# Performance work log

Measured on AMD Instinct MI355X. Metric: run time of the kernel, lower is better.

## Reference

```python
import jax, jax.numpy as jnp
import numpy as np

B, S, HID, NH, DH, L, FF = 1, 4096, 768, 12, 64, 12, 3072
WIN = 256       # one-sided sliding window (attention_window = 512 total)
NG = 16         # number of global-attention tokens
VOCAB = 50265
NEG = -1e9


def layer_norm(x, g, b, eps=1e-5):
    mu = jnp.mean(x, -1, keepdims=True)
    var = jnp.mean((x - mu) ** 2, -1, keepdims=True)
    return (x - mu) * jax.lax.rsqrt(var + eps) * g + b


def forward(input_ids, attention_mask, global_attention_mask, tok_emb, pos_emb,
            emb_ln_w, emb_ln_b, Wqkv, bqkv, Wo, bo, ln1_w, ln1_b,
            W1, b1, W2, b2, ln2_w, ln2_b, cls_W, cls_b):
    c = WIN
    nc = S // c
    amask = attention_mask.astype(jnp.float32)          # [B,S]
    gmask = global_attention_mask.astype(jnp.float32)   # [B,S]

    # --- static-shape helpers for the sparse pattern ---
    # key chunk k covers padded positions [k*c, k*c + 3c)
    idx = (jnp.arange(nc) * c)[:, None] + jnp.arange(3 * c)[None, :]      # [nc,3c]
    diff = jnp.arange(3 * c)[None, :] - c - jnp.arange(c)[:, None]        # [c,3c]
    band = jnp.abs(diff) <= c
    mp = jnp.pad(amask, ((0, 0), (c, c)))[:, idx]                         # [B,nc,3c]
    gp = jnp.pad(gmask, ((0, 0), (c, c)))[:, idx]
    key_ok = (mp > 0) & (gp == 0)           # local keys: valid and not global (globals handled separately)
    loc_valid = band[None, None] & key_ok[:, :, None, :]                  # [B,nc,c,3c]

    # indices of the NG global tokens (earliest first)
    _, gidx = jax.lax.top_k(gmask * (2.0 * S) - jnp.arange(S, dtype=jnp.float32), NG)
    gvalid = jnp.take_along_axis(gmask, gidx, axis=1)                     # [B,NG]

    def attn(x, Wqkv_l, bqkv_l, Wo_l, bo_l):
        qkv = x @ Wqkv_l + bqkv_l
        q, k, v = jnp.split(qkv, 3, axis=-1)
        hd = lambda t: t.reshape(B, S, NH, DH).transpose(0, 2, 1, 3)      # [B,nh,S,dh]
        q = hd(q) * (DH ** -0.5); k = hd(k); v = hd(v)

        # sliding-window (banded) attention via overlapping key chunks
        kp = jnp.pad(k, ((0, 0), (0, 0), (c, c), (0, 0)))
        vp = jnp.pad(v, ((0, 0), (0, 0), (c, c), (0, 0)))
        Kc, Vc = kp[:, :, idx], vp[:, :, idx]                             # [B,nh,nc,3c,dh]
        Qc = q.reshape(B, NH, nc, c, DH)
        s_loc = jnp.einsum('bhkpd,bhkqd->bhkpq', Qc, Kc)                  # [B,nh,nc,c,3c]
        s_loc = jnp.where(loc_valid[:, None], s_loc, NEG)

        # every token also attends to the global tokens
        gi = jnp.broadcast_to(gidx[:, None, :, None], (B, NH, NG, DH))
        Kg = jnp.take_along_axis(k, gi, axis=2)                           # [B,nh,NG,dh]
        Vg = jnp.take_along_axis(v, gi, axis=2)
        Qg = jnp.take_along_axis(q, gi, axis=2)
        s_glb = jnp.einsum('bhkpd,bhgd->bhkpg', Qc, Kg)                   # [B,nh,nc,c,NG]
        s_glb = jnp.where(gvalid[:, None, None, None, :] > 0, s_glb, NEG)

        p = jax.nn.softmax(jnp.concatenate([s_loc, s_glb], -1), axis=-1)
        o = (jnp.einsum('bhkpq,bhkqd->bhkpd', p[..., :3 * c], Vc)
             + jnp.einsum('bhkpg,bhgd->bhkpd', p[..., 3 * c:], Vg))
        o = o.reshape(B, NH, S, DH).transpose(0, 2, 1, 3)                 # [B,S,nh,dh]

        # global tokens attend to the full sequence
        s_full = jnp.einsum('bhgd,bhsd->bhgs', Qg, k)
        s_full = jnp.where(amask[:, None, None, :] > 0, s_full, NEG)
        og = jnp.einsum('bhgs,bhsd->bhgd', jax.nn.softmax(s_full, -1), v)
        og = og.transpose(0, 2, 1, 3)                                     # [B,NG,nh,dh]
        bi = jnp.arange(B)[:, None]
        o = o.at[bi, gidx].set(jnp.where(gvalid[..., None, None] > 0, og, o[bi, gidx]))
        return o.reshape(B, S, HID) @ Wo_l + bo_l

    h = layer_norm(tok_emb[input_ids] + pos_emb[None], emb_ln_w, emb_ln_b)

    def step(h, p):
        Wq, bq, Wo_l, bo_l, g1, bl1, w1, bb1, w2, bb2, g2, bl2 = p
        h = layer_norm(h + attn(h, Wq, bq, Wo_l, bo_l), g1, bl1)          # post-LN, RoBERTa-style
        f = jax.nn.gelu(h @ w1 + bb1, approximate=False) @ w2 + bb2
        h = layer_norm(h + f, g2, bl2)
        return h, None

    h, _ = jax.lax.scan(step, h, (Wqkv, bqkv, Wo, bo, ln1_w, ln1_b,
                                  W1, b1, W2, b2, ln2_w, ln2_b))
    m = amask[..., None]
    pooled = (h * m).sum(1) / m.sum(1)           # masked mean-pool; dropout is eval no-op
    return pooled @ cls_W + cls_b                # [B,2] logits


def setup_inputs():
    key = jax.random.key(0)
    ks = jax.random.split(key, 8)
    nrm = lambda k, shp: jax.random.normal(k, shp, jnp.float32) * 0.02
    return dict(
        input_ids=jax.random.randint(ks[0], (B, S), 0, VOCAB),
        attention_mask=jnp.ones((B, S), jnp.int32),
        global_attention_mask=jnp.concatenate(
            [jnp.ones((B, NG), jnp.int32), jnp.zeros((B, S - NG), jnp.int32)], axis=1),
        tok_emb=nrm(ks[1], (VOCAB, HID)),
        pos_emb=nrm(ks[2], (S, HID)),
        emb_ln_w=jnp.ones((HID,)), emb_ln_b=jnp.zeros((HID,)),
        Wqkv=nrm(ks[3], (L, HID, 3 * HID)), bqkv=jnp.zeros((L, 3 * HID)),
        Wo=nrm(ks[4], (L, HID, HID)), bo=jnp.zeros((L, HID)),
        ln1_w=jnp.ones((L, HID)), ln1_b=jnp.zeros((L, HID)),
        W1=nrm(ks[5], (L, HID, FF)), b1=jnp.zeros((L, FF)),
        W2=nrm(ks[6], (L, FF, HID)), b2=jnp.zeros((L, HID)),
        ln2_w=jnp.ones((L, HID)), ln2_b=jnp.zeros((L, HID)),
        cls_W=nrm(ks[7], (HID, 2)), cls_b=jnp.zeros((2,)),
    )


def reference(input_ids, attention_mask, global_attention_mask, tok_emb, pos_emb,
              emb_ln_w, emb_ln_b, Wqkv, bqkv, Wo, bo, ln1_w, ln1_b,
              W1, b1, W2, b2, ln2_w, ln2_b, cls_W, cls_b):
    return forward(input_ids, attention_mask, global_attention_mask, tok_emb, pos_emb,
                   emb_ln_w, emb_ln_b, Wqkv, bqkv, Wo, bo, ln1_w, ln1_b,
                   W1, b1, W2, b2, ln2_w, ln2_b, cls_W, cls_b)
```

## Files before the change

### kernel.cpp

```cpp
#include <hip/hip_runtime.h>
#include <cmath>

#define S 4096
#define HID 768
#define NH 12
#define DH 64
#define CHUNK 256
#define NC (S / CHUNK)
#define NG 16
#define FF 3072
#define NLAYER 12
#define QKV3 (3 * HID)
#define NEGV -1e9f

typedef _Float16 f16;
typedef __attribute__((ext_vector_type(2))) _Float16 f16x2;
typedef __attribute__((ext_vector_type(4))) _Float16 f16x4;
typedef __attribute__((ext_vector_type(8))) _Float16 f16x8;
typedef __attribute__((ext_vector_type(4))) float f32x4;

__device__ __forceinline__ void async16(f16* lds, const f16* g) {
  __builtin_amdgcn_global_load_lds((const __attribute__((address_space(1))) unsigned int*)g,
                                   (__attribute__((address_space(3))) unsigned int*)lds,
                                   16, 0, 0);
}

__device__ __forceinline__ int xcd_swz(int lin, int nwg) {
  return (lin & 7) * (nwg >> 3) + (lin >> 3);
}

__device__ __forceinline__ float block_reduce_sum(float v, float* red) {
  int t = threadIdx.x;
  red[t] = v; __syncthreads();
  for (int st = 128; st > 0; st >>= 1) {
    if (t < st) red[t] += red[t + st];
    __syncthreads();
  }
  float r = red[0]; __syncthreads();
  return r;
}

__global__ void gidx_kernel(const int* __restrict__ gmask, int* __restrict__ gidx,
                            float* __restrict__ gvalid) {
  if (threadIdx.x != 0 || blockIdx.x != 0) return;
  int cnt = 0;
  for (int s = 0; s < S && cnt < NG; s++)
    if (gmask[s] > 0) { gidx[cnt] = s; gvalid[cnt] = 1.f; cnt++; }
  for (int s = 0; s < S && cnt < NG; s++)
    if (gmask[s] == 0) { gidx[cnt] = s; gvalid[cnt] = 0.f; cnt++; }
}

__global__ __launch_bounds__(256) void embed_ln_kernel(
    const int* __restrict__ ids, const float* __restrict__ tok,
    const float* __restrict__ pos, const float* __restrict__ g,
    const float* __restrict__ b, f16* __restrict__ h16) {
  int s = blockIdx.x, t = threadIdx.x;
  __shared__ float xs[HID];
  __shared__ float red[256];
  const float* tr = tok + (size_t)ids[s] * HID;
  const float* pr = pos + (size_t)s * HID;
  float ls = 0.f;
  for (int i = t; i < HID; i += 256) { float v = tr[i] + pr[i]; xs[i] = v; ls += v; }
  float mu = block_reduce_sum(ls, red) * (1.f / HID);
  float lv = 0.f;
  for (int i = t; i < HID; i += 256) { float d = xs[i] - mu; lv += d * d; }
  float var = block_reduce_sum(lv, red) * (1.f / HID);
  float inv = rsqrtf(var + 1e-5f);
  for (int i = t; i < HID; i += 256)
    h16[(size_t)s * HID + i] = (f16)((xs[i] - mu) * inv * g[i] + b[i]);
}

__global__ __launch_bounds__(256) void ln_kernel(
    const f16* __restrict__ sum16, const float* __restrict__ g,
    const float* __restrict__ b, f16* __restrict__ h16) {
  int s = blockIdx.x, t = threadIdx.x;
  __shared__ float red[256];
  float x[4] = {0.f, 0.f, 0.f, 0.f};
  if (t < 192) {
    f16x4 v = *(const f16x4*)&sum16[(size_t)s * HID + t * 4];
#pragma unroll
    for (int e = 0; e < 4; e++) x[e] = (float)v[e];
  }
  float mu = block_reduce_sum(x[0] + x[1] + x[2] + x[3], red) * (1.f / HID);
  float vs = 0.f;
  if (t < 192) {
#pragma unroll
    for (int e = 0; e < 4; e++) { float d = x[e] - mu; vs += d * d; }
  }
  float var = block_reduce_sum(vs, red) * (1.f / HID);
  float inv = rsqrtf(var + 1e-5f);
  if (t < 192) {
    float4 gv = *(const float4*)&g[t * 4];
    float4 bv = *(const float4*)&b[t * 4];
    f16x4 o;
    o[0] = (f16)((x[0] - mu) * inv * gv.x + bv.x);
    o[1] = (f16)((x[1] - mu) * inv * gv.y + bv.y);
    o[2] = (f16)((x[2] - mu) * inv * gv.z + bv.z);
    o[3] = (f16)((x[3] - mu) * inv * gv.w + bv.w);
    *(f16x4*)&h16[(size_t)s * HID + t * 4] = o;
  }
}

__global__ __launch_bounds__(256) void ln_ffn2_kernel(
    const f16* __restrict__ p0, const f16* __restrict__ p1,
    const float* __restrict__ bias, const float* __restrict__ g,
    const float* __restrict__ b, f16* __restrict__ h16) {
  int s = blockIdx.x, t = threadIdx.x;
  __shared__ float red[256];
  size_t base = (size_t)s * HID;
  float x[4] = {0.f, 0.f, 0.f, 0.f};
  if (t < 192) {
    f16x4 a = *(const f16x4*)&p0[base + t * 4];
    f16x4 c = *(const f16x4*)&p1[base + t * 4];
    f16x4 r = *(const f16x4*)&h16[base + t * 4];
    float4 bb = *(const float4*)&bias[t * 4];
    x[0] = (float)a[0] + (float)c[0] + bb.x + (float)r[0];
    x[1] = (float)a[1] + (float)c[1] + bb.y + (float)r[1];
    x[2] = (float)a[2] + (float)c[2] + bb.z + (float)r[2];
    x[3] = (float)a[3] + (float)c[3] + bb.w + (float)r[3];
  }
  float mu = block_reduce_sum(x[0] + x[1] + x[2] + x[3], red) * (1.f / HID);
  float vs = 0.f;
  if (t < 192) {
#pragma unroll
    for (int e = 0; e < 4; e++) { float d = x[e] - mu; vs += d * d; }
  }
  float var = block_reduce_sum(vs, red) * (1.f / HID);
  float inv = rsqrtf(var + 1e-5f);
  if (t < 192) {
    float4 gv = *(const float4*)&g[t * 4];
    float4 bv = *(const float4*)&b[t * 4];
    f16x4 o;
    o[0] = (f16)((x[0] - mu) * inv * gv.x + bv.x);
    o[1] = (f16)((x[1] - mu) * inv * gv.y + bv.y);
    o[2] = (f16)((x[2] - mu) * inv * gv.z + bv.z);
    o[3] = (f16)((x[3] - mu) * inv * gv.w + bv.w);
    *(f16x4*)&h16[base + t * 4] = o;
  }
}

__global__ __launch_bounds__(256) void wt_kernel(const float* __restrict__ W,
                                                 f16* __restrict__ WT, int K, int N) {
  size_t lo = (size_t)blockIdx.z * K * N;
  const float* Wl = W + lo;
  f16* WTl = WT + lo;
  __shared__ float tile[32][33];
  int k0 = blockIdx.y * 32, n0 = blockIdx.x * 32;
  int t = threadIdx.x;
  int r = t >> 3, c = (t & 7) * 4;
  float4 v = *(const float4*)&Wl[(size_t)(k0 + r) * N + n0 + c];
  tile[r][c] = v.x; tile[r][c + 1] = v.y; tile[r][c + 2] = v.z; tile[r][c + 3] = v.w;
  __syncthreads();
  int n = t >> 3, kq = (t & 7) * 4;
  f16x4 o = {(f16)tile[kq][n], (f16)tile[kq + 1][n], (f16)tile[kq + 2][n], (f16)tile[kq + 3][n]};
  *(f16x4*)&WTl[(size_t)(n0 + n) * K + k0 + kq] = o;
}

#define GBK 64

template <bool GELU>
__global__ __launch_bounds__(256) void gemm_f16_kernel(
    const f16* __restrict__ A, const f16* __restrict__ BT,
    const float* __restrict__ bias, f16* __restrict__ Cout, int M, int N, int K) {
  __shared__ f16 smem[17408];
  f16* As = smem;
  f16* Bs = smem + 8192;
  int t = threadIdx.x, lane = t & 63, wave = t >> 6;
  int wr = wave >> 1, wc = wave & 1;
  int gx = gridDim.x;
  int nl = xcd_swz(blockIdx.y * gx + blockIdx.x, gx * gridDim.y);
  int bx = nl % gx, by = nl / gx;

  f32x4 acc[4][4];
#pragma unroll
  for (int mi = 0; mi < 4; mi++)
#pragma unroll
    for (int ni = 0; ni < 4; ni++) acc[mi][ni] = (f32x4){0.f, 0.f, 0.f, 0.f};

  const f16* Ablk = A + (size_t)(by * 128) * K;
  const f16* Bblk = BT + (size_t)(bx * 128) * K;
  int rl = lane >> 3;
  int lc = (lane & 7) ^ rl;

  for (int k0 = 0; k0 < K; k0 += GBK) {
#pragma unroll
    for (int ii = 0; ii < 4; ii++) {
      int i = wave * 4 + ii;
      int r = i * 8 + rl;
      async16(&As[i * 512], Ablk + (size_t)r * K + k0 + lc * 8);
      async16(&Bs[i * 512], Bblk + (size_t)r * K + k0 + lc * 8);
    }
    __syncthreads();
#pragma unroll
    for (int kc = 0; kc < 2; kc++) {
      f16x8 af[4], bf[4];
#pragma unroll
      for (int mi = 0; mi < 4; mi++) {
        int row = wr * 64 + mi * 16 + (lane & 15);
        int pc = (kc * 4 + (lane >> 4)) ^ (row & 7);
        af[mi] = *(const f16x8*)&As[row * 64 + pc * 8];
      }
#pragma unroll
      for (int ni = 0; ni < 4; ni++) {
        int row = wc * 64 + ni * 16 + (lane & 15);
        int pc = (kc * 4 + (lane >> 4)) ^ (row & 7);
        bf[ni] = *(const f16x8*)&Bs[row * 64 + pc * 8];
      }
#pragma unroll
      for (int mi = 0; mi < 4; mi++)
#pragma unroll
        for (int ni = 0; ni < 4; ni++)
          acc[mi][ni] = __builtin_amdgcn_mfma_f32_16x16x32_f16(af[mi], bf[ni], acc[mi][ni], 0, 0, 0);
    }
    __syncthreads();
  }

  f16* Cs = smem;
  int rloc = wr * 64 + (lane >> 4) * 4;
  int cloc = wc * 64 + (lane & 15);
#pragma unroll
  for (int mi = 0; mi < 4; mi++) {
#pragma unroll
    for (int ni = 0; ni < 4; ni++) {
      int col = cloc + ni * 16;
      float bs = bias[bx * 128 + col];
#pragma unroll
      for (int j = 0; j < 4; j++) {
        float x = acc[mi][ni][j] + bs;
        if (GELU) x = 0.5f * x * (1.f + erff(x * 0.70710678118654752f));
        Cs[(rloc + mi * 16 + j) * 136 + col] = (f16)x;
      }
    }
  }
  __syncthreads();
  size_t Cb = (size_t)(by * 128) * N + bx * 128;
#pragma unroll
  for (int p = 0; p < 8; p++) {
    int idx = p * 256 + t;
    int row = idx >> 4, ch = idx & 15;
    f16x8 v = *(const f16x8*)&Cs[row * 136 + ch * 8];
    *(f16x8*)&Cout[Cb + (size_t)row * N + ch * 8] = v;
  }
}

template <bool RESID>
__global__ __launch_bounds__(256) void gemm_f16_n64_kernel(
    const f16* __restrict__ A, const f16* __restrict__ BT,
    const float* __restrict__ bias, const f16* __restrict__ resid,
    f16* __restrict__ Cout, int M, int N, int K) {
  __shared__ f16 smem[12288];
  f16* As = smem;
  f16* Bs = smem + 8192;
  int t = threadIdx.x, lane = t & 63, wave = t >> 6;
  int wr = wave >> 1, wc = wave & 1;
  int gx = gridDim.x;
  int nl = xcd_swz(blockIdx.y * gx + blockIdx.x, gx * gridDim.y);
  int bx = nl % gx, by = nl / gx;

  f32x4 acc[4][2];
#pragma unroll
  for (int mi = 0; mi < 4; mi++)
#pragma unroll
    for (int ni = 0; ni < 2; ni++) acc[mi][ni] = (f32x4){0.f, 0.f, 0.f, 0.f};

  const f16* Ablk = A + (size_t)(by * 128) * K;
  const f16* Bblk = BT + (size_t)(bx * 64) * K;
  int rl = lane >> 3;
  int lc = (lane & 7) ^ rl;

  for (int k0 = 0; k0 < K; k0 += GBK) {
#pragma unroll
    for (int ii = 0; ii < 4; ii++) {
      int i = wave * 4 + ii;
      int r = i * 8 + rl;
      async16(&As[i * 512], Ablk + (size_t)r * K + k0 + lc * 8);
    }
#pragma unroll
    for (int ii = 0; ii < 2; ii++) {
      int i = wave * 2 + ii;
      int r = i * 8 + rl;
      async16(&Bs[i * 512], Bblk + (size_t)r * K + k0 + lc * 8);
    }
    __syncthreads();
#pragma unroll
    for (int kc = 0; kc < 2; kc++) {
      f16x8 af[4], bf[2];
#pragma unroll
      for (int mi = 0; mi < 4; mi++) {
        int row = wr * 64 + mi * 16 + (lane & 15);
        int pc = (kc * 4 + (lane >> 4)) ^ (row & 7);
        af[mi] = *(const f16x8*)&As[row * 64 + pc * 8];
      }
#pragma unroll
      for (int ni = 0; ni < 2; ni++) {
        int row = wc * 32 + ni * 16 + (lane & 15);
        int pc = (kc * 4 + (lane >> 4)) ^ (row & 7);
        bf[ni] = *(const f16x8*)&Bs[row * 64 + pc * 8];
      }
#pragma unroll
      for (int mi = 0; mi < 4; mi++)
#pragma unroll
        for (int ni = 0; ni < 2; ni++)
          acc[mi][ni] = __builtin_amdgcn_mfma_f32_16x16x32_f16(af[mi], bf[ni], acc[mi][ni], 0, 0, 0);
    }
    __syncthreads();
  }

  f16* Cs = smem;
  int rloc = wr * 64 + (lane >> 4) * 4;
  int cloc = wc * 32 + (lane & 15);
#pragma unroll
  for (int mi = 0; mi < 4; mi++) {
#pragma unroll
    for (int ni = 0; ni < 2; ni++) {
      int col = cloc + ni * 16;
      float bs = bias[bx * 64 + col];
#pragma unroll
      for (int j = 0; j < 4; j++)
        Cs[(rloc + mi * 16 + j) * 72 + col] = (f16)(acc[mi][ni][j] + bs);
    }
  }
  __syncthreads();
  size_t Cb = (size_t)(by * 128) * N + bx * 64;
#pragma unroll
  for (int p = 0; p < 4; p++) {
    int idx = p * 256 + t;
    int row = idx >> 3, ch = idx & 7;
    f16x8 v = *(const f16x8*)&Cs[row * 72 + ch * 8];
    if (RESID) {
      f16x8 r = *(const f16x8*)&resid[Cb + (size_t)row * N + ch * 8];
#pragma unroll
      for (int e = 0; e < 8; e++) v[e] = (f16)((float)v[e] + (float)r[e]);
    }
    *(f16x8*)&Cout[Cb + (size_t)row * N + ch * 8] = v;
  }
}

__global__ __launch_bounds__(256) void gemm_f16_n64_splitk_kernel(
    const f16* __restrict__ A, const f16* __restrict__ BT,
    f16* __restrict__ p0, f16* __restrict__ p1, int M, int N, int K) {
  __shared__ f16 smem[12288];
  f16* As = smem;
  f16* Bs = smem + 8192;
  int t = threadIdx.x, lane = t & 63, wave = t >> 6;
  int wr = wave >> 1, wc = wave & 1;
  int gx = gridDim.x;
  int nl = xcd_swz(blockIdx.y * gx + blockIdx.x, gx * gridDim.y);
  int bx = nl % gx, by = nl / gx;
  int kz = blockIdx.z;
  int KH = K >> 1;
  f16* pout = kz ? p1 : p0;

  f32x4 acc[4][2];
#pragma unroll
  for (int mi = 0; mi < 4; mi++)
#pragma unroll
    for (int ni = 0; ni < 2; ni++) acc[mi][ni] = (f32x4){0.f, 0.f, 0.f, 0.f};

  const f16* Ablk = A + (size_t)(by * 128) * K + (size_t)kz * KH;
  const f16* Bblk = BT + (size_t)(bx * 64) * K + (size_t)kz * KH;
  int rl = lane >> 3;
  int lc = (lane & 7) ^ rl;

  for (int k0 = 0; k0 < KH; k0 += GBK) {
#pragma unroll
    for (int ii = 0; ii < 4; ii++) {
      int i = wave * 4 + ii;
      int r = i * 8 + rl;
      async16(&As[i * 512], Ablk + (size_t)r * K + k0 + lc * 8);
    }
#pragma unroll
    for (int ii = 0; ii < 2; ii++) {
      int i = wave * 2 + ii;
      int r = i * 8 + rl;
      async16(&Bs[i * 512], Bblk + (size_t)r * K + k0 + lc * 8);
    }
    __syncthreads();
#pragma unroll
    for (int kc = 0; kc < 2; kc++) {
      f16x8 af[4], bf[2];
#pragma unroll
      for (int mi = 0; mi < 4; mi++) {
        int row = wr * 64 + mi * 16 + (lane & 15);
        int pc = (kc * 4 + (lane >> 4)) ^ (row & 7);
        af[mi] = *(const f16x8*)&As[row * 64 + pc * 8];
      }
#pragma unroll
      for (int ni = 0; ni < 2; ni++) {
        int row = wc * 32 + ni * 16 + (lane & 15);
        int pc = (kc * 4 + (lane >> 4)) ^ (row & 7);
        bf[ni] = *(const f16x8*)&Bs[row * 64 + pc * 8];
      }
#pragma unroll
      for (int mi = 0; mi < 4; mi++)
#pragma unroll
        for (int ni = 0; ni < 2; ni++)
          acc[mi][ni] = __builtin_amdgcn_mfma_f32_16x16x32_f16(af[mi], bf[ni], acc[mi][ni], 0, 0, 0);
    }
    __syncthreads();
  }

  f16* Cs = smem;
  int rloc = wr * 64 + (lane >> 4) * 4;
  int cloc = wc * 32 + (lane & 15);
#pragma unroll
  for (int mi = 0; mi < 4; mi++)
#pragma unroll
    for (int ni = 0; ni < 2; ni++)
#pragma unroll
      for (int j = 0; j < 4; j++)
        Cs[(rloc + mi * 16 + j) * 72 + cloc + ni * 16] = (f16)acc[mi][ni][j];
  __syncthreads();
  size_t Cb = (size_t)(by * 128) * N + bx * 64;
#pragma unroll
  for (int p = 0; p < 4; p++) {
    int idx = p * 256 + t;
    int row = idx >> 3, ch = idx & 7;
    f16x8 v = *(const f16x8*)&Cs[row * 72 + ch * 8];
    *(f16x8*)&pout[Cb + (size_t)row * N + ch * 8] = v;
  }
}

#define ROWP 72

__device__ __forceinline__ void pf_load(
    const f16* __restrict__ qkv, const int* __restrict__ gidx, const float* gvs,
    int h, int q0, int kt, int t,
    f16x8& pk0, f16x8& pk1, f16x8& pva, f16x8& pvb) {
  int jb = q0 - 256 + kt * 64;
  bool isG = (kt == 9);
  pk0 = (f16x8){}; pk1 = (f16x8){}; pva = (f16x8){}; pvb = (f16x8){};
  int kr = t >> 2, c2 = (t & 3) * 2;
  bool kok_;
  int jk;
  if (isG) { kok_ = (kr < NG) && (gvs[kr] > 0.f); jk = kok_ ? gidx[kr] : 0; }
  else { kok_ = true; jk = jb + kr; }
  if (kok_) {
    const f16* kp = qkv + (size_t)jk * QKV3 + HID + h * DH + c2 * 8;
    pk0 = *(const f16x8*)kp;
    pk1 = *(const f16x8*)(kp + 8);
  }
  int k2 = (t & 31) * 2, dq = (t >> 5) * 8;
  bool o0, o1;
  int j0, j1;
  if (isG) {
    o0 = (k2 < NG) && (gvs[k2] > 0.f); j0 = o0 ? gidx[k2] : 0;
    o1 = (k2 + 1 < NG) && (gvs[k2 + 1] > 0.f); j1 = o1 ? gidx[k2 + 1] : 0;
  } else { o0 = o1 = true; j0 = jb + k2; j1 = jb + k2 + 1; }
  if (o0) pva = *(const f16x8*)(qkv + (size_t)j0 * QKV3 + 2 * HID + h * DH + dq);
  if (o1) pvb = *(const f16x8*)(qkv + (size_t)j1 * QKV3 + 2 * HID + h * DH + dq);
}

__global__ __launch_bounds__(256) void local_attn_mfma_kernel(
    const f16* __restrict__ qkv, const int* __restrict__ amask,
    const int* __restrict__ gmask, const int* __restrict__ gidx,
    const float* __restrict__ gvalid, f16* __restrict__ outp) {
  int nl = xcd_swz(blockIdx.x, NH * 64);
  int h = nl >> 6;
  int qb = nl & 63;
  int q0 = qb * 64;
  int t = threadIdx.x, lane = t & 63, w = t >> 6;
  int g4 = lane >> 4, l15 = lane & 15;

  __shared__ f16 Qs[64 * ROWP];
  __shared__ f16 Kt[64 * ROWP];
  __shared__ f16 Vt[64 * ROWP];
  __shared__ f16 Pb[4 * 16 * ROWP];
  __shared__ unsigned kokLo, kokHi;
  __shared__ float gvs[NG];

  {
    int r = t >> 2, c2 = (t & 3) * 2;
    const f16* qr = qkv + (size_t)(q0 + r) * QKV3 + h * DH + c2 * 8;
    f16x8 v0 = *(const f16x8*)qr;
    f16x8 v1 = *(const f16x8*)(qr + 8);
#pragma unroll
    for (int e = 0; e < 8; e++) { v0[e] = v0[e] * (f16)0.125f; v1[e] = v1[e] * (f16)0.125f; }
    *(f16x8*)&Qs[r * ROWP + c2 * 8] = v0;
    *(f16x8*)&Qs[r * ROWP + c2 * 8 + 8] = v1;
    if (t < NG) gvs[t] = gvalid[t];
  }
  __syncthreads();

  int qrow = w * 16 + l15;
  f16x8 qf0 = *(const f16x8*)&Qs[qrow * ROWP + g4 * 8];
  f16x8 qf1 = *(const f16x8*)&Qs[qrow * ROWP + 32 + g4 * 8];

  float mb = -50000.f, lp = 0.f;
  f32x4 oacc[4];
#pragma unroll
  for (int sd = 0; sd < 4; sd++) oacc[sd] = (f32x4){0.f, 0.f, 0.f, 0.f};

  f16* Pw = &Pb[w * 16 * ROWP];

  int kt_lo = q0 >= 256 ? 0 : (256 - q0) >> 6;
  int kt_hi = (4288 - q0) >> 6;
  if (kt_hi > 8) kt_hi = 8;
  int ntile = kt_hi - kt_lo + 2;

  f16x8 pk0, pk1, pva, pvb;
  pf_load(qkv, gidx, gvs, h, q0, kt_lo, t, pk0, pk1, pva, pvb);

  for (int it = 0; it < ntile; it++) {
    int kt = (it < ntile - 1) ? kt_lo + it : 9;
    int jb = q0 - 256 + kt * 64;
    bool isG = (kt == 9);
    __syncthreads();
    {
      int kr = t >> 2, c2 = (t & 3) * 2;
      *(f16x8*)&Kt[kr * ROWP + c2 * 8] = pk0;
      *(f16x8*)&Kt[kr * ROWP + c2 * 8 + 8] = pk1;
    }
    {
      int k2 = (t & 31) * 2, dq = (t >> 5) * 8;
#pragma unroll
      for (int e = 0; e < 8; e++) {
        f16x2 pr = {pva[e], pvb[e]};
        *(f16x2*)&Vt[(dq + e) * ROWP + k2] = pr;
      }
    }
    if (w == 0) {
      int k = lane;
      bool ok;
      if (isG) ok = (k < NG && gvs[k] > 0.f);
      else {
        int j = jb + k;
        ok = (amask[j] != 0) && (gmask[j] == 0);
      }
      unsigned long long m = __ballot(ok);
      if (lane == 0) { kokLo = (unsigned)m; kokHi = (unsigned)(m >> 32); }
    }
    if (it + 1 < ntile) {
      int ktn = (it + 1 < ntile - 1) ? kt_lo + it + 1 : 9;
      pf_load(qkv, gidx, gvs, h, q0, ktn, t, pk0, pk1, pva, pvb);
    }
    __syncthreads();

    unsigned long long kok = ((unsigned long long)kokHi << 32) | (unsigned long long)kokLo;

    f32x4 sv[4];
    __builtin_amdgcn_s_setprio(1);
#pragma unroll
    for (int s4 = 0; s4 < 4; s4++) {
      int krow = s4 * 16 + l15;
      f16x8 ka0 = *(const f16x8*)&Kt[krow * ROWP + g4 * 8];
      f16x8 ka1 = *(const f16x8*)&Kt[krow * ROWP + 32 + g4 * 8];
      f32x4 a = {0.f, 0.f, 0.f, 0.f};
      a = __builtin_amdgcn_mfma_f32_16x16x32_f16(ka0, qf0, a, 0, 0, 0);
      a = __builtin_amdgcn_mfma_f32_16x16x32_f16(ka1, qf1, a, 0, 0, 0);
      sv[s4] = a;
    }
    __builtin_amdgcn_s_setprio(0);
    int ql = w * 16 + l15;
#pragma unroll
    for (int s4 = 0; s4 < 4; s4++)
#pragma unroll
      for (int r = 0; r < 4; r++) {
        int kl = s4 * 16 + g4 * 4 + r;
        bool ok = (kok >> kl) & 1ull;
        if (kt == 0) ok = ok && (kl >= ql);
        else if (kt == 8) ok = ok && (kl <= ql);
        sv[s4][r] = ok ? sv[s4][r] : -1e30f;
      }
    float mt = -1e30f;
#pragma unroll
    for (int s4 = 0; s4 < 4; s4++)
#pragma unroll
      for (int r = 0; r < 4; r++) mt = fmaxf(mt, sv[s4][r]);
    mt = fmaxf(mt, __shfl_xor(mt, 16));
    mt = fmaxf(mt, __shfl_xor(mt, 32));
    float mn = fmaxf(mb, mt);
    float corr = __expf(mb - mn);
    mb = mn;
    lp *= corr;
#pragma unroll
    for (int sd = 0; sd < 4; sd++)
#pragma unroll
      for (int r = 0; r < 4; r++) oacc[sd][r] *= corr;
#pragma unroll
    for (int s4 = 0; s4 < 4; s4++) {
#pragma unroll
      for (int rp = 0; rp < 2; rp++) {
        float p0 = __expf(sv[s4][rp * 2] - mn);
        float p1 = __expf(sv[s4][rp * 2 + 1] - mn);
        f16 h0 = (f16)p0, h1 = (f16)p1;
        lp += (float)h0 + (float)h1;
        int kl = s4 * 16 + g4 * 4 + rp * 2;
        f16x2 pr = {h0, h1};
        *(f16x2*)&Pw[l15 * ROWP + kl] = pr;
      }
    }
    f16x8 pf0 = *(const f16x8*)&Pw[l15 * ROWP + g4 * 8];
    f16x8 pf1 = *(const f16x8*)&Pw[l15 * ROWP + 32 + g4 * 8];
    __builtin_amdgcn_s_setprio(1);
#pragma unroll
    for (int sd = 0; sd < 4; sd++) {
      int drow = sd * 16 + l15;
      f16x8 va0 = *(const f16x8*)&Vt[drow * ROWP + g4 * 8];
      f16x8 va1 = *(const f16x8*)&Vt[drow * ROWP + 32 + g4 * 8];
      oacc[sd] = __builtin_amdgcn_mfma_f32_16x16x32_f16(va0, pf0, oacc[sd], 0, 0, 0);
      oacc[sd] = __builtin_amdgcn_mfma_f32_16x16x32_f16(va1, pf1, oacc[sd], 0, 0, 0);
    }
    __builtin_amdgcn_s_setprio(0);
  }

  float lt = lp + __shfl_xor(lp, 16);
  lt = lt + __shfl_xor(lt, 32);
  float inv = (lt > 0.f) ? 1.f / lt : 0.f;
  int qg = q0 + w * 16 + l15;
  f16* orow = outp + (size_t)qg * HID + h * DH;
#pragma unroll
  for (int sd = 0; sd < 4; sd++)
#pragma unroll
    for (int r = 0; r < 4; r++)
      orow[sd * 16 + g4 * 4 + r] = (f16)(oacc[sd][r] * inv);
}

__global__ __launch_bounds__(256) void gscore_kernel(
    const f16* __restrict__ qkv, const int* __restrict__ amask,
    const int* __restrict__ gidx, float* __restrict__ Sg, float2* __restrict__ cstat) {
  int h = blockIdx.x >> 4, jc = blockIdx.x & 15;
  int t = threadIdx.x, lane = t & 63, w = t >> 6;
  __shared__ f16 Qs[NG][DH];
  __shared__ float wred[4][NG];
  __shared__ float cmaxs[NG];
  if (t < 128) {
    int g = t >> 3, c = (t & 7) * 8;
    const f16* qr = qkv + (size_t)gidx[g] * QKV3 + h * DH + c;
    *(f16x8*)&Qs[g][c] = *(const f16x8*)qr;
  }
  __syncthreads();
  int j = jc * 256 + t;
  const f16x8* kr = (const f16x8*)(qkv + (size_t)j * QKV3 + HID + h * DH);
  f16x8 kv[8];
#pragma unroll
  for (int c = 0; c < 8; c++) kv[c] = kr[c];
  bool ok = amask[j] != 0;
  float sg[NG];
#pragma unroll 4
  for (int g = 0; g < NG; g++) {
    float s = 0.f;
#pragma unroll
    for (int c = 0; c < 8; c++) {
      f16x8 qv = *(const f16x8*)&Qs[g][c * 8];
#pragma unroll
      for (int e = 0; e < 8; e++) s += (float)qv[e] * (float)kv[c][e];
    }
    sg[g] = ok ? s * 0.125f : NEGV;
    Sg[(size_t)(h * NG + g) * S + j] = sg[g];
  }
#pragma unroll
  for (int g = 0; g < NG; g++) {
    float m = sg[g];
#pragma unroll
    for (int st = 1; st < 64; st <<= 1) m = fmaxf(m, __shfl_xor(m, st));
    if (lane == 0) wred[w][g] = m;
  }
  __syncthreads();
  if (t < NG)
    cmaxs[t] = fmaxf(fmaxf(wred[0][t], wred[1][t]), fmaxf(wred[2][t], wred[3][t]));
  __syncthreads();
#pragma unroll
  for (int g = 0; g < NG; g++) {
    float p = __expf(sg[g] - cmaxs[g]);
#pragma unroll
    for (int st = 1; st < 64; st <<= 1) p += __shfl_xor(p, st);
    if (lane == 0) wred[w][g] = p;
  }
  __syncthreads();
  if (t < NG) {
    float s4 = wred[0][t] + wred[1][t] + wred[2][t] + wred[3][t];
    cstat[((size_t)(h * NG + t)) * 16 + jc] = make_float2(cmaxs[t], s4);
  }
}

__global__ __launch_bounds__(256) void gpv_kernel(
    const f16* __restrict__ qkv, const float* __restrict__ Sg,
    const float2* __restrict__ cstat, float* __restrict__ part) {
  int h = blockIdx.x >> 4, jc = blockIdx.x & 15;
  int jb = jc * 256;
  int t = threadIdx.x;
  __shared__ float Ps[NG][256];
  __shared__ f16 Vs[256][DH];
  __shared__ float ms[NG], dinv[NG];
  if (t < NG) {
    const float2* cs = &cstat[((size_t)(h * NG + t)) * 16];
    float m = -1e30f;
#pragma unroll
    for (int c = 0; c < 16; c++) m = fmaxf(m, cs[c].x);
    float den = 0.f;
#pragma unroll
    for (int c = 0; c < 16; c++) den += cs[c].y * __expf(cs[c].x - m);
    ms[t] = m;
    dinv[t] = den > 0.f ? 1.f / den : 0.f;
  }
  __syncthreads();
#pragma unroll
  for (int g = 0; g < NG; g++)
    Ps[g][t] = __expf(Sg[(size_t)(h * NG + g) * S + jb + t] - ms[g]) * dinv[g];
  {
    int r = t >> 3, c = (t & 7) * 8;
#pragma unroll
    for (int pp = 0; pp < 8; pp++) {
      int row = pp * 32 + r;
      const f16* vr = qkv + (size_t)(jb + row) * QKV3 + 2 * HID + h * DH + c;
      *(f16x8*)&Vs[row][c] = *(const f16x8*)vr;
    }
  }
  __syncthreads();
  int d = t & 63, g4 = t >> 6;
  float o0 = 0.f, o1 = 0.f, o2 = 0.f, o3 = 0.f;
#pragma unroll 8
  for (int j = 0; j < 256; j++) {
    float v = (float)Vs[j][d];
    o0 += Ps[g4][j] * v;
    o1 += Ps[g4 + 4][j] * v;
    o2 += Ps[g4 + 8][j] * v;
    o3 += Ps[g4 + 12][j] * v;
  }
  size_t base = ((size_t)h * NG) * 16 * 64;
  part[base + ((size_t)(g4) * 16 + jc) * 64 + d] = o0;
  part[base + ((size_t)(g4 + 4) * 16 + jc) * 64 + d] = o1;
  part[base + ((size_t)(g4 + 8) * 16 + jc) * 64 + d] = o2;
  part[base + ((size_t)(g4 + 12) * 16 + jc) * 64 + d] = o3;
}

__global__ __launch_bounds__(64) void gout_kernel(
    const float* __restrict__ part, const int* __restrict__ gidx,
    const float* __restrict__ gvalid, f16* __restrict__ attn16) {
  int h = blockIdx.x >> 4, g = blockIdx.x & 15;
  if (gvalid[g] <= 0.f) return;
  int d = threadIdx.x;
  const float* pr = part + (((size_t)(h * NG + g)) * 16) * 64 + d;
  float s = 0.f;
#pragma unroll
  for (int jc = 0; jc < 16; jc++) s += pr[jc * 64];
  attn16[(size_t)gidx[g] * HID + h * DH + d] = (f16)s;
}

__global__ __launch_bounds__(256) void pool_part_kernel(
    const f16* __restrict__ h, const int* __restrict__ amask, float* __restrict__ part) {
  int b = blockIdx.x, t = threadIdx.x;
  if (t >= 192) return;
  float a[4] = {0.f, 0.f, 0.f, 0.f};
  for (int r = 0; r < 64; r++) {
    int s = b * 64 + r;
    float w = (float)amask[s];
    f16x4 v = *(const f16x4*)&h[(size_t)s * HID + t * 4];
#pragma unroll
    for (int e = 0; e < 4; e++) a[e] += (float)v[e] * w;
  }
  float4 o = {a[0], a[1], a[2], a[3]};
  *(float4*)&part[(size_t)b * HID + t * 4] = o;
}

__global__ __launch_bounds__(256) void cls_head_kernel(
    const float* __restrict__ part, const int* __restrict__ amask,
    const float* __restrict__ clsW, const float* __restrict__ clsb,
    float* __restrict__ out) {
  __shared__ float pooled[HID];
  __shared__ float red[256];
  int t = threadIdx.x;
  for (int i = t; i < HID; i += 256) {
    float s = 0.f;
    for (int b2 = 0; b2 < 64; b2++) s += part[(size_t)b2 * HID + i];
    pooled[i] = s;
  }
  float c = 0.f;
  for (int s2 = t; s2 < S; s2 += 256) c += (float)amask[s2];
  float cnt = block_reduce_sum(c, red);
  float p0 = 0.f, p1 = 0.f;
  for (int i = t; i < HID; i += 256) {
    float pv = pooled[i] / cnt;
    p0 += pv * clsW[i * 2];
    p1 += pv * clsW[i * 2 + 1];
  }
  float s0 = block_reduce_sum(p0, red);
  float s1 = block_reduce_sum(p1, red);
  if (t == 0) { out[0] = s0 + clsb[0]; out[1] = s1 + clsb[1]; }
}

extern "C" void kernel_launch(void* const* d_in, const int* in_sizes, int n_in,
                              void* d_out, int out_size, void* d_ws, size_t ws_size,
                              hipStream_t stream) {
  const int* ids = (const int*)d_in[0];
  const int* amask = (const int*)d_in[1];
  const int* gmask = (const int*)d_in[2];
  const float* tok = (const float*)d_in[3];
  const float* pos = (const float*)d_in[4];
  const float* elnw = (const float*)d_in[5];
  const float* elnb = (const float*)d_in[6];
  const float* Wqkv = (const float*)d_in[7];
  const float* bqkv = (const float*)d_in[8];
  const float* Wo = (const float*)d_in[9];
  const float* bo = (const float*)d_in[10];
  const float* ln1w = (const float*)d_in[11];
  const float* ln1b = (const float*)d_in[12];
  const float* W1 = (const float*)d_in[13];
  const float* b1 = (const float*)d_in[14];
  const float* W2 = (const float*)d_in[15];
  const float* b2 = (const float*)d_in[16];
  const float* ln2w = (const float*)d_in[17];
  const float* ln2b = (const float*)d_in[18];
  const float* clsW = (const float*)d_in[19];
  const float* clsb = (const float*)d_in[20];

  char* w8 = (char*)d_ws;
  size_t o = 0;
  f16* h16 = (f16*)(w8 + o); o += (size_t)S * HID * 2;
  f16* qkv16 = (f16*)(w8 + o); o += (size_t)S * QKV3 * 2;
  f16* attn16 = (f16*)(w8 + o); o += (size_t)S * HID * 2;
  f16* ff16 = (f16*)(w8 + o); o += (size_t)S * FF * 2;
  f16* sum16 = (f16*)(w8 + o); o += (size_t)S * HID * 2;
  f16* p1 = (f16*)(w8 + o); o += (size_t)S * HID * 2;
  float* part = (float*)(w8 + o); o += (size_t)64 * HID * 4;
  int* gidx = (int*)(w8 + o); o += 64;
  float* gvalid = (float*)(w8 + o); o += 64;
  f16* WqkvT = (f16*)(w8 + o); o += (size_t)NLAYER * HID * QKV3 * 2;
  f16* WoT = (f16*)(w8 + o); o += (size_t)NLAYER * HID * HID * 2;
  f16* W1T = (f16*)(w8 + o); o += (size_t)NLAYER * HID * FF * 2;
  f16* W2T = (f16*)(w8 + o); o += (size_t)NLAYER * FF * HID * 2;
  float* Sg = (float*)(w8 + o); o += (size_t)NH * NG * S * 4;
  float2* cstat = (float2*)(w8 + o); o += (size_t)NH * NG * 16 * 8;
  float* gpart = (float*)(w8 + o); o += (size_t)NH * NG * 16 * 64 * 4;

  gidx_kernel<<<1, 64, 0, stream>>>(gmask, gidx, gvalid);
  embed_ln_kernel<<<S, 256, 0, stream>>>(ids, tok, pos, elnw, elnb, h16);
  wt_kernel<<<dim3(QKV3 / 32, HID / 32, NLAYER), 256, 0, stream>>>(Wqkv, WqkvT, HID, QKV3);
  wt_kernel<<<dim3(HID / 32, HID / 32, NLAYER), 256, 0, stream>>>(Wo, WoT, HID, HID);
  wt_kernel<<<dim3(FF / 32, HID / 32, NLAYER), 256, 0, stream>>>(W1, W1T, HID, FF);
  wt_kernel<<<dim3(HID / 32, FF / 32, NLAYER), 256, 0, stream>>>(W2, W2T, FF, HID);

  for (int l = 0; l < NLAYER; l++) {
    gemm_f16_kernel<false><<<dim3(QKV3 / 128, S / 128), 256, 0, stream>>>(
        h16, WqkvT + (size_t)l * HID * QKV3, bqkv + (size_t)l * QKV3, qkv16, S, QKV3, HID);
    local_attn_mfma_kernel<<<NH * 64, 256, 0, stream>>>(
        qkv16, amask, gmask, gidx, gvalid, attn16);
    gscore_kernel<<<NH * 16, 256, 0, stream>>>(qkv16, amask, gidx, Sg, cstat);
    gpv_kernel<<<NH * 16, 256, 0, stream>>>(qkv16, Sg, cstat, gpart);
    gout_kernel<<<NH * NG, 64, 0, stream>>>(gpart, gidx, gvalid, attn16);
    gemm_f16_n64_kernel<true><<<dim3(HID / 64, S / 128), 256, 0, stream>>>(
        attn16, WoT + (size_t)l * HID * HID, bo + (size_t)l * HID, h16, sum16, S, HID, HID);
    ln_kernel<<<S, 256, 0, stream>>>(sum16, ln1w + (size_t)l * HID, ln1b + (size_t)l * HID, h16);
    gemm_f16_kernel<true><<<dim3(FF / 128, S / 128), 256, 0, stream>>>(
        h16, W1T + (size_t)l * HID * FF, b1 + (size_t)l * FF, ff16, S, FF, HID);
    gemm_f16_n64_splitk_kernel<<<dim3(HID / 64, S / 128, 2), 256, 0, stream>>>(
        ff16, W2T + (size_t)l * FF * HID, sum16, p1, S, HID, FF);
    ln_ffn2_kernel<<<S, 256, 0, stream>>>(sum16, p1, b2 + (size_t)l * HID,
                                          ln2w + (size_t)l * HID, ln2b + (size_t)l * HID, h16);
  }
  pool_part_kernel<<<64, 256, 0, stream>>>(h16, amask, part);
  cls_head_kernel<<<1, 256, 0, stream>>>(part, amask, clsW, clsb, (float*)d_out);
}
```

Baseline: 2.321 ms.

## Double-buffer GEMM LDS tiles with BK=32 to overlap async loads with MFMA

All three f16 GEMM kernels switch from a single-buffered BK=64 loop to a double-buffered BK=32 pipeline. The next K-slice is issued via async global-to-LDS loads before the MFMAs on the current slice, with a matching XOR swizzle for 32-wide rows. The goal is to hide global load latency behind compute and halve the barriers per unit of prefetch. The risk is that the smaller K-step doubles the loop iterations and barrier count, and that async loads may not have landed when only one __syncthreads separates the stages.

```diff
diff --git a/kernel.cpp b/kernel.cpp
--- a/kernel.cpp
+++ b/kernel.cpp
@@ -156,7 +156,6 @@
   *(f16x4*)&WTl[(size_t)(n0 + n) * K + k0 + kq] = o;
 }
 
-#define GBK 64
 
 template <bool GELU>
 __global__ __launch_bounds__(256) void gemm_f16_kernel(
@@ -179,41 +178,48 @@
 
   const f16* Ablk = A + (size_t)(by * 128) * K;
   const f16* Bblk = BT + (size_t)(bx * 128) * K;
-  int rl = lane >> 3;
-  int lc = (lane & 7) ^ rl;
-
-  for (int k0 = 0; k0 < K; k0 += GBK) {
-#pragma unroll
-    for (int ii = 0; ii < 4; ii++) {
-      int i = wave * 4 + ii;
-      int r = i * 8 + rl;
-      async16(&As[i * 512], Ablk + (size_t)r * K + k0 + lc * 8);
-      async16(&Bs[i * 512], Bblk + (size_t)r * K + k0 + lc * 8);
-    }
+  int srow = lane >> 2;
+  int sch = lane & 3;
+
+#define STAGE128(b, k0)                                                        \
+  {                                                                            \
+    _Pragma("unroll") for (int ii = 0; ii < 2; ii++) {                         \
+      int blk = wave * 2 + ii;                                                 \
+      int row = blk * 16 + srow;                                               \
+      int sc = sch ^ ((row >> 1) & 3);                                         \
+      async16(&As[(b) * 4096 + blk * 512], Ablk + (size_t)row * K + (k0) + sc * 8); \
+      async16(&Bs[(b) * 4096 + blk * 512], Bblk + (size_t)row * K + (k0) + sc * 8); \
+    }                                                                          \
+  }
+
+  int nt = K >> 5;
+  STAGE128(0, 0);
+  __syncthreads();
+  int cur = 0;
+  for (int tt = 0; tt < nt; tt++) {
+    if (tt + 1 < nt) STAGE128(cur ^ 1, (tt + 1) * 32);
+    f16x8 af[4], bf[4];
+#pragma unroll
+    for (int mi = 0; mi < 4; mi++) {
+      int row = wr * 64 + mi * 16 + (lane & 15);
+      int pc = (lane >> 4) ^ ((row >> 1) & 3);
+      af[mi] = *(const f16x8*)&As[cur * 4096 + row * 32 + pc * 8];
+    }
+#pragma unroll
+    for (int ni = 0; ni < 4; ni++) {
+      int row = wc * 64 + ni * 16 + (lane & 15);
+      int pc = (lane >> 4) ^ ((row >> 1) & 3);
+      bf[ni] = *(const f16x8*)&Bs[cur * 4096 + row * 32 + pc * 8];
+    }
+#pragma unroll
+    for (int mi = 0; mi < 4; mi++)
+#pragma unroll
+      for (int ni = 0; ni < 4; ni++)
+        acc[mi][ni] = __builtin_amdgcn_mfma_f32_16x16x32_f16(af[mi], bf[ni], acc[mi][ni], 0, 0, 0);
     __syncthreads();
-#pragma unroll
-    for (int kc = 0; kc < 2; kc++) {
-      f16x8 af[4], bf[4];
-#pragma unroll
-      for (int mi = 0; mi < 4; mi++) {
-        int row = wr * 64 + mi * 16 + (lane & 15);
-        int pc = (kc * 4 + (lane >> 4)) ^ (row & 7);
-        af[mi] = *(const f16x8*)&As[row * 64 + pc * 8];
-      }
-#pragma unroll
-      for (int ni = 0; ni < 4; ni++) {
-        int row = wc * 64 + ni * 16 + (lane & 15);
-        int pc = (kc * 4 + (lane >> 4)) ^ (row & 7);
-        bf[ni] = *(const f16x8*)&Bs[row * 64 + pc * 8];
-      }
-#pragma unroll
-      for (int mi = 0; mi < 4; mi++)
-#pragma unroll
-        for (int ni = 0; ni < 4; ni++)
-          acc[mi][ni] = __builtin_amdgcn_mfma_f32_16x16x32_f16(af[mi], bf[ni], acc[mi][ni], 0, 0, 0);
-    }
-    __syncthreads();
-  }
+    cur ^= 1;
+  }
+#undef STAGE128
 
   f16* Cs = smem;
   int rloc = wr * 64 + (lane >> 4) * 4;
@@ -265,46 +271,52 @@
 
   const f16* Ablk = A + (size_t)(by * 128) * K;
   const f16* Bblk = BT + (size_t)(bx * 64) * K;
-  int rl = lane >> 3;
-  int lc = (lane & 7) ^ rl;
-
-  for (int k0 = 0; k0 < K; k0 += GBK) {
-#pragma unroll
-    for (int ii = 0; ii < 4; ii++) {
-      int i = wave * 4 + ii;
-      int r = i * 8 + rl;
-      async16(&As[i * 512], Ablk + (size_t)r * K + k0 + lc * 8);
-    }
-#pragma unroll
-    for (int ii = 0; ii < 2; ii++) {
-      int i = wave * 2 + ii;
-      int r = i * 8 + rl;
-      async16(&Bs[i * 512], Bblk + (size_t)r * K + k0 + lc * 8);
-    }
+  int srow = lane >> 2;
+  int sch = lane & 3;
+
+#define STAGE64(b, k0)                                                         \
+  {                                                                            \
+    _Pragma("unroll") for (int ii = 0; ii < 2; ii++) {                         \
+      int blk = wave * 2 + ii;                                                 \
+      int row = blk * 16 + srow;                                               \
+      int sc = sch ^ ((row >> 1) & 3);                                         \
+      async16(&As[(b) * 4096 + blk * 512], Ablk + (size_t)row * K + (k0) + sc * 8); \
+    }                                                                          \
+    {                                                                          \
+      int row = wave * 16 + srow;                                              \
+      int sc = sch ^ ((row >> 1) & 3);                                         \
+      async16(&Bs[(b) * 2048 + wave * 512], Bblk + (size_t)row * K + (k0) + sc * 8); \
+    }                                                                          \
+  }
+
+  int nt = K >> 5;
+  STAGE64(0, 0);
+  __syncthreads();
+  int cur = 0;
+  for (int tt = 0; tt < nt; tt++) {
+    if (tt + 1 < nt) STAGE64(cur ^ 1, (tt + 1) * 32);
+    f16x8 af[4], bf[2];
+#pragma unroll
+    for (int mi = 0; mi < 4; mi++) {
+      int row = wr * 64 + mi * 16 + (lane & 15);
+      int pc = (lane >> 4) ^ ((row >> 1) & 3);
+      af[mi] = *(const f16x8*)&As[cur * 4096 + row * 32 + pc * 8];
+    }
+#pragma unroll
+    for (int ni = 0; ni < 2; ni++) {
+      int row = wc * 32 + ni * 16 + (lane & 15);
+      int pc = (lane >> 4) ^ ((row >> 1) & 3);
+      bf[ni] = *(const f16x8*)&Bs[cur * 2048 + row * 32 + pc * 8];
+    }
+#pragma unroll
+    for (int mi = 0; mi < 4; mi++)
+#pragma unroll
+      for (int ni = 0; ni < 2; ni++)
+        acc[mi][ni] = __builtin_amdgcn_mfma_f32_16x16x32_f16(af[mi], bf[ni], acc[mi][ni], 0, 0, 0);
     __syncthreads();
-#pragma unroll
-    for (int kc = 0; kc < 2; kc++) {
-      f16x8 af[4], bf[2];
-#pragma unroll
-      for (int mi = 0; mi < 4; mi++) {
-        int row = wr * 64 + mi * 16 + (lane & 15);
-        int pc = (kc * 4 + (lane >> 4)) ^ (row & 7);
-        af[mi] = *(const f16x8*)&As[row * 64 + pc * 8];
-      }
-#pragma unroll
-      for (int ni = 0; ni < 2; ni++) {
-        int row = wc * 32 + ni * 16 + (lane & 15);
-        int pc = (kc * 4 + (lane >> 4)) ^ (row & 7);
-        bf[ni] = *(const f16x8*)&Bs[row * 64 + pc * 8];
-      }
-#pragma unroll
-      for (int mi = 0; mi < 4; mi++)
-#pragma unroll
-        for (int ni = 0; ni < 2; ni++)
-          acc[mi][ni] = __builtin_amdgcn_mfma_f32_16x16x32_f16(af[mi], bf[ni], acc[mi][ni], 0, 0, 0);
-    }
-    __syncthreads();
-  }
+    cur ^= 1;
+  }
+#undef STAGE64
 
   f16* Cs = smem;
   int rloc = wr * 64 + (lane >> 4) * 4;
@@ -359,46 +371,52 @@
 
   const f16* Ablk = A + (size_t)(by * 128) * K + (size_t)kz * KH;
   const f16* Bblk = BT + (size_t)(bx * 64) * K + (size_t)kz * KH;
-  int rl = lane >> 3;
-  int lc = (lane & 7) ^ rl;
-
-  for (int k0 = 0; k0 < KH; k0 += GBK) {
-#pragma unroll
-    for (int ii = 0; ii < 4; ii++) {
-      int i = wave * 4 + ii;
-      int r = i * 8 + rl;
-      async16(&As[i * 512], Ablk + (size_t)r * K + k0 + lc * 8);
-    }
-#pragma unroll
-    for (int ii = 0; ii < 2; ii++) {
-      int i = wave * 2 + ii;
-      int r = i * 8 + rl;
-      async16(&Bs[i * 512], Bblk + (size_t)r * K + k0 + lc * 8);
-    }
+  int srow = lane >> 2;
+  int sch = lane & 3;
+
+#define STAGESK(b, k0)                                                         \
+  {                                                                            \
+    _Pragma("unroll") for (int ii = 0; ii < 2; ii++) {                         \
+      int blk = wave * 2 + ii;                                                 \
+      int row = blk * 16 + srow;                                               \
+      int sc = sch ^ ((row >> 1) & 3);                                         \
+      async16(&As[(b) * 4096 + blk * 512], Ablk + (size_t)row * K + (k0) + sc * 8); \
+    }                                                                          \
+    {                                                                          \
+      int row = wave * 16 + srow;                                              \
+      int sc = sch ^ ((row >> 1) & 3);                                         \
+      async16(&Bs[(b) * 2048 + wave * 512], Bblk + (size_t)row * K + (k0) + sc * 8); \
+    }                                                                          \
+  }
+
+  int nt = KH >> 5;
+  STAGESK(0, 0);
+  __syncthreads();
+  int cur = 0;
+  for (int tt = 0; tt < nt; tt++) {
+    if (tt + 1 < nt) STAGESK(cur ^ 1, (tt + 1) * 32);
+    f16x8 af[4], bf[2];
+#pragma unroll
+    for (int mi = 0; mi < 4; mi++) {
+      int row = wr * 64 + mi * 16 + (lane & 15);
+      int pc = (lane >> 4) ^ ((row >> 1) & 3);
+      af[mi] = *(const f16x8*)&As[cur * 4096 + row * 32 + pc * 8];
+    }
+#pragma unroll
+    for (int ni = 0; ni < 2; ni++) {
+      int row = wc * 32 + ni * 16 + (lane & 15);
+      int pc = (lane >> 4) ^ ((row >> 1) & 3);
+      bf[ni] = *(const f16x8*)&Bs[cur * 2048 + row * 32 + pc * 8];
+    }
+#pragma unroll
+    for (int mi = 0; mi < 4; mi++)
+#pragma unroll
+      for (int ni = 0; ni < 2; ni++)
+        acc[mi][ni] = __builtin_amdgcn_mfma_f32_16x16x32_f16(af[mi], bf[ni], acc[mi][ni], 0, 0, 0);
     __syncthreads();
-#pragma unroll
-    for (int kc = 0; kc < 2; kc++) {
-      f16x8 af[4], bf[2];
-#pragma unroll
-      for (int mi = 0; mi < 4; mi++) {
-        int row = wr * 64 + mi * 16 + (lane & 15);
-        int pc = (kc * 4 + (lane >> 4)) ^ (row & 7);
-        af[mi] = *(const f16x8*)&As[row * 64 + pc * 8];
-      }
-#pragma unroll
-      for (int ni = 0; ni < 2; ni++) {
-        int row = wc * 32 + ni * 16 + (lane & 15);
-        int pc = (kc * 4 + (lane >> 4)) ^ (row & 7);
-        bf[ni] = *(const f16x8*)&Bs[row * 64 + pc * 8];
-      }
-#pragma unroll
-      for (int mi = 0; mi < 4; mi++)
-#pragma unroll
-        for (int ni = 0; ni < 2; ni++)
-          acc[mi][ni] = __builtin_amdgcn_mfma_f32_16x16x32_f16(af[mi], bf[ni], acc[mi][ni], 0, 0, 0);
-    }
-    __syncthreads();
-  }
+    cur ^= 1;
+  }
+#undef STAGESK
 
   f16* Cs = smem;
   int rloc = wr * 64 + (lane >> 4) * 4;
```

Result: slower. 2.387 ms (+2.8%).
